# Performance work log

Measured on AMD Instinct MI355X. Metric: run time of the kernel, lower is better.

## Reference

```python
import jax, jax.numpy as jnp
import numpy as np

F_DIM = 14
E_DIM = 64
H1 = E_DIM // 4   # 16
H2 = E_DIM // 2   # 32
H3 = E_DIM // 4   # 16
LN_EPS = 1e-5


def setup_inputs() -> dict:
    key = jax.random.key(0)
    ks = jax.random.split(key, 12)
    B, N = 4, 100000
    x = jax.random.normal(ks[0], (B, N, F_DIM), dtype=jnp.float32)
    # LayerNorm(1) params per feature (torch init: weight=1, bias=0)
    gamma = jnp.ones((F_DIM,), jnp.float32)
    beta = jnp.zeros((F_DIM,), jnp.float32)
    # Stacked per-feature MLP weights: Linear(1,H1)->GELU->Linear(H1,H2)->GELU->Linear(H2,H3)->GELU->Linear(H3,E)
    W1 = jax.random.normal(ks[1], (F_DIM, 1, H1), jnp.float32) * 0.02
    b1 = jnp.zeros((F_DIM, H1), jnp.float32)
    W2 = jax.random.normal(ks[2], (F_DIM, H1, H2), jnp.float32) * 0.02
    b2 = jnp.zeros((F_DIM, H2), jnp.float32)
    W3 = jax.random.normal(ks[3], (F_DIM, H2, H3), jnp.float32) * 0.02
    b3 = jnp.zeros((F_DIM, H3), jnp.float32)
    W4 = jax.random.normal(ks[4], (F_DIM, H3, E_DIM), jnp.float32) * 0.02
    b4 = jnp.zeros((F_DIM, E_DIM), jnp.float32)
    # param type embeddings, init normal std=0.02
    emb = jax.random.normal(ks[5], (F_DIM, E_DIM), jnp.float32) * 0.02
    return {"x": x, "gamma": gamma, "beta": beta, "W1": W1, "b1": b1,
            "W2": W2, "b2": b2, "W3": W3, "b3": b3, "W4": W4, "b4": b4,
            "emb": emb}


def reference(x, gamma, beta, W1, b1, W2, b2, W3, b3, W4, b4, emb):
    B, N, F = x.shape
    # LayerNorm over a singleton dim: mean = x, var = 0 -> normalized = 0,
    # so output = 0 * gamma + beta (faithful to torch LayerNorm(1)).
    normed = (x - x) / jnp.sqrt(jnp.asarray(LN_EPS, x.dtype)) * gamma + beta  # [B,N,F]
    gelu = lambda t: jax.nn.gelu(t, approximate=False)
    h = gelu(normed[..., None] * W1[:, 0, :] + b1)          # [B,N,F,H1]
    h = gelu(jnp.einsum('bnfh,fhk->bnfk', h, W2) + b2)      # [B,N,F,H2]
    h = gelu(jnp.einsum('bnfh,fhk->bnfk', h, W3) + b3)      # [B,N,F,H3]
    out = jnp.einsum('bnfh,fhe->bnfe', h, W4) + b4 + emb    # [B,N,F,E]
    # torch.cat over features along last dim == reshape of [B,N,F,E]
    return out.reshape(B, N, F * out.shape[-1])
```

## Files before the change

### kernel.cpp

```cpp
#include <hip/hip_runtime.h>
#include <hip/hip_bf16.h>

#define F_DIM 14
#define H1D 16
#define H2D 32
#define H3D 16
#define E_DIM 64

__device__ __forceinline__ float gelu_exact(float x) {
    return 0.5f * x * (1.0f + erff(x * 0.70710678118654752440f));
}

__global__ void build_table_kernel(const float* __restrict__ beta,
                                   const float* __restrict__ W1,
                                   const float* __restrict__ b1,
                                   const float* __restrict__ W2,
                                   const float* __restrict__ b2,
                                   const float* __restrict__ W3,
                                   const float* __restrict__ b3,
                                   const float* __restrict__ W4,
                                   const float* __restrict__ b4,
                                   const float* __restrict__ emb,
                                   float* __restrict__ table) {
    const int tid = (int)threadIdx.x;
    const int f = tid >> 6;
    const int e = tid & 63;
    if (f >= F_DIM) return;

    const float v = beta[f];

    float h1[H1D], h2[H2D], h3[H3D];
    #pragma unroll
    for (int k = 0; k < H1D; ++k)
        h1[k] = gelu_exact(v * W1[f * H1D + k] + b1[f * H1D + k]);

    #pragma unroll
    for (int j = 0; j < H2D; ++j) {
        float acc = b2[f * H2D + j];
        #pragma unroll
        for (int k = 0; k < H1D; ++k)
            acc += h1[k] * W2[(f * H1D + k) * H2D + j];
        h2[j] = gelu_exact(acc);
    }

    #pragma unroll
    for (int j = 0; j < H3D; ++j) {
        float acc = b3[f * H3D + j];
        #pragma unroll
        for (int k = 0; k < H2D; ++k)
            acc += h2[k] * W3[(f * H2D + k) * H3D + j];
        h3[j] = gelu_exact(acc);
    }

    float acc = b4[f * E_DIM + e] + emb[f * E_DIM + e];
    #pragma unroll
    for (int m = 0; m < H3D; ++m)
        acc += h3[m] * W4[(f * H3D + m) * E_DIM + e];

    table[tid] = acc;
}

__global__ __launch_bounds__(256) void broadcast_kernel(const float4* __restrict__ table4,
                                                        float4* __restrict__ out4,
                                                        int total4) {
    const int stride = (int)(gridDim.x * blockDim.x);
    int idx = (int)(blockIdx.x * blockDim.x + threadIdx.x);
    const int c = idx % 224;
    const float4 tv = table4[c];
    for (; idx < total4; idx += stride)
        out4[idx] = tv;
}

extern "C" void kernel_launch(void* const* d_in, const int* in_sizes, int n_in,
                              void* d_out, int out_size, void* d_ws, size_t ws_size,
                              hipStream_t stream) {
    const float* beta = (const float*)d_in[2];
    const float* W1   = (const float*)d_in[3];
    const float* b1   = (const float*)d_in[4];
    const float* W2   = (const float*)d_in[5];
    const float* b2   = (const float*)d_in[6];
    const float* W3   = (const float*)d_in[7];
    const float* b3   = (const float*)d_in[8];
    const float* W4   = (const float*)d_in[9];
    const float* b4   = (const float*)d_in[10];
    const float* emb  = (const float*)d_in[11];

    float* out = (float*)d_out;

    float* table = (ws_size >= (size_t)(F_DIM * E_DIM * sizeof(float)))
                       ? (float*)d_ws : out;

    build_table_kernel<<<1, F_DIM * E_DIM, 0, stream>>>(
        beta, W1, b1, W2, b2, W3, b3, W4, b4, emb, table);

    const int total4 = out_size / 4;
    const int blocks = 3584;
    broadcast_kernel<<<blocks, 256, 0, stream>>>(
        (const float4*)table, (float4*)out, total4);
}
```

Baseline: 1.444 ms.

## Fuse table build into broadcast kernel with per-block recompute and nontemporal stores

Removes the separate single-block table-building launch. Each block of the broadcast grid now recomputes the tiny per-feature MLP table into shared memory and then writes it out. Stores use nontemporal hints, and the grid doubles from 3584 to 7168 blocks. This cuts a kernel launch and its serialization. In exchange every block redoes the small MLP with erf calls, which adds a serial prologue per block before the store-bound loop starts.

New measurement: 1.551 ms. +7.4%, slower.

```diff
diff --git a/kernel.cpp b/kernel.cpp
--- a/kernel.cpp
+++ b/kernel.cpp
@@ -6,69 +6,75 @@
 #define H2D 32
 #define H3D 16
 #define E_DIM 64
+#define TBL   896
+#define TBL4  224
+#define BLOCK 256
+#define GRID  7168
+
+typedef float vfloat4 __attribute__((ext_vector_type(4)));
+
 
 __device__ __forceinline__ float gelu_exact(float x) {
     return 0.5f * x * (1.0f + erff(x * 0.70710678118654752440f));
 }
 
-__global__ void build_table_kernel(const float* __restrict__ beta,
-                                   const float* __restrict__ W1,
-                                   const float* __restrict__ b1,
-                                   const float* __restrict__ W2,
-                                   const float* __restrict__ b2,
-                                   const float* __restrict__ W3,
-                                   const float* __restrict__ b3,
-                                   const float* __restrict__ W4,
-                                   const float* __restrict__ b4,
-                                   const float* __restrict__ emb,
-                                   float* __restrict__ table) {
+__global__ __launch_bounds__(BLOCK) void fused_bcast_kernel(
+        const float* __restrict__ beta,
+        const float* __restrict__ W1, const float* __restrict__ b1,
+        const float* __restrict__ W2, const float* __restrict__ b2,
+        const float* __restrict__ W3, const float* __restrict__ b3,
+        const float* __restrict__ W4, const float* __restrict__ b4,
+        const float* __restrict__ emb,
+        vfloat4* __restrict__ out4, int total4) {
+    __shared__ float h3s[F_DIM][H3D];
+    __shared__ vfloat4 table4[TBL4];
+
     const int tid = (int)threadIdx.x;
-    const int f = tid >> 6;
-    const int e = tid & 63;
-    if (f >= F_DIM) return;
 
-    const float v = beta[f];
-
-    float h1[H1D], h2[H2D], h3[H3D];
-    #pragma unroll
-    for (int k = 0; k < H1D; ++k)
-        h1[k] = gelu_exact(v * W1[f * H1D + k] + b1[f * H1D + k]);
-
-    #pragma unroll
-    for (int j = 0; j < H2D; ++j) {
-        float acc = b2[f * H2D + j];
+    if (tid < F_DIM) {
+        const int f = tid;
+        const float v = beta[f];
+        float h1[H1D], h2[H2D];
         #pragma unroll
         for (int k = 0; k < H1D; ++k)
-            acc += h1[k] * W2[(f * H1D + k) * H2D + j];
-        h2[j] = gelu_exact(acc);
+            h1[k] = gelu_exact(v * W1[f * H1D + k] + b1[f * H1D + k]);
+        #pragma unroll
+        for (int j = 0; j < H2D; ++j) {
+            float acc = b2[f * H2D + j];
+            #pragma unroll
+            for (int k = 0; k < H1D; ++k)
+                acc += h1[k] * W2[(f * H1D + k) * H2D + j];
+            h2[j] = gelu_exact(acc);
+        }
+        #pragma unroll
+        for (int j = 0; j < H3D; ++j) {
+            float acc = b3[f * H3D + j];
+            #pragma unroll
+            for (int k = 0; k < H2D; ++k)
+                acc += h2[k] * W3[(f * H2D + k) * H3D + j];
+            h3s[f][j] = gelu_exact(acc);
+        }
     }
+    __syncthreads();
 
-    #pragma unroll
-    for (int j = 0; j < H3D; ++j) {
-        float acc = b3[f * H3D + j];
+    float* table = (float*)table4;
+    for (int g = tid; g < TBL; g += BLOCK) {
+        const int f = g >> 6;
+        const int e = g & 63;
+        float acc = b4[g] + emb[g];
         #pragma unroll
-        for (int k = 0; k < H2D; ++k)
-            acc += h2[k] * W3[(f * H2D + k) * H3D + j];
-        h3[j] = gelu_exact(acc);
+        for (int m = 0; m < H3D; ++m)
+            acc += h3s[f][m] * W4[(f * H3D + m) * E_DIM + e];
+        table[g] = acc;
     }
+    __syncthreads();
 
-    float acc = b4[f * E_DIM + e] + emb[f * E_DIM + e];
-    #pragma unroll
-    for (int m = 0; m < H3D; ++m)
-        acc += h3[m] * W4[(f * H3D + m) * E_DIM + e];
-
-    table[tid] = acc;
-}
-
-__global__ __launch_bounds__(256) void broadcast_kernel(const float4* __restrict__ table4,
-                                                        float4* __restrict__ out4,
-                                                        int total4) {
-    const int stride = (int)(gridDim.x * blockDim.x);
-    int idx = (int)(blockIdx.x * blockDim.x + threadIdx.x);
-    const int c = idx % 224;
-    const float4 tv = table4[c];
+    int idx = (int)(blockIdx.x * BLOCK + tid);
+    const int c = idx % TBL4;
+    const vfloat4 tv = table4[c];
+    const int stride = GRID * BLOCK;
     for (; idx < total4; idx += stride)
-        out4[idx] = tv;
+        __builtin_nontemporal_store(tv, &out4[idx]);
 }
 
 extern "C" void kernel_launch(void* const* d_in, const int* in_sizes, int n_in,
@@ -85,16 +91,8 @@
     const float* b4   = (const float*)d_in[10];
     const float* emb  = (const float*)d_in[11];
 
-    float* out = (float*)d_out;
-
-    float* table = (ws_size >= (size_t)(F_DIM * E_DIM * sizeof(float)))
-                       ? (float*)d_ws : out;
-
-    build_table_kernel<<<1, F_DIM * E_DIM, 0, stream>>>(
-        beta, W1, b1, W2, b2, W3, b3, W4, b4, emb, table);
-
     const int total4 = out_size / 4;
-    const int blocks = 3584;
-    broadcast_kernel<<<blocks, 256, 0, stream>>>(
-        (const float4*)table, (float4*)out, total4);
+    fused_bcast_kernel<<<GRID, BLOCK, 0, stream>>>(
+        beta, W1, b1, W2, b2, W3, b3, W4, b4, emb,
+        (vfloat4*)d_out, total4);
 }
```
